# Performance work log

Measured on AMD Instinct MI355X. Metric: run time of the kernel, lower is better.

## Reference

```python
import jax, jax.numpy as jnp
import numpy as np

WS = 3          # window size (odd)
NH = 8          # num heads
EPS = 1e-5      # LayerNorm eps (torch default)


def _ln(x, g, b):
    mu = x.mean(-1, keepdims=True)
    var = ((x - mu) ** 2).mean(-1, keepdims=True)
    return (x - mu) / jnp.sqrt(var + EPS) * g + b


def _neighbors(x, ws):
    # x: [B,D,H,W,C] -> [B,D,H,W,ws^3,C] zero-padded cubic neighborhoods
    B, D, H, W, C = x.shape
    r = ws // 2
    xp = jnp.pad(x, ((0, 0), (r, r), (r, r), (r, r), (0, 0)))
    slabs = [xp[:, i:i + D, j:j + H, k:k + W, :]
             for i in range(ws) for j in range(ws) for k in range(ws)]
    return jnp.stack(slabs, axis=4)


def _mask(D, H, W, ws):
    # True for valid (in-bounds, non-center) neighbors: [D,H,W,ws^3]
    r = ws // 2
    valid = jnp.pad(jnp.ones((D, H, W), dtype=bool), ((r, r), (r, r), (r, r)))
    slabs = [valid[i:i + D, j:j + H, k:k + W]
             for i in range(ws) for j in range(ws) for k in range(ws)]
    m = jnp.stack(slabs, axis=3)
    center = r * ws * ws + r * ws + r  # self voxel is masked out
    return m.at[..., center].set(False)


def setup_inputs() -> dict:
    key = jax.random.key(0)
    ks = jax.random.split(key, 18)
    B, D, H, W, C = 2, 16, 16, 16, 256
    F = 4 * C
    s = 0.02
    inp = {
        "x": jax.random.normal(ks[0], (B, D, H, W, C), jnp.float32),
        "Wq": jax.random.normal(ks[1], (C, C), jnp.float32) * s,
        "bq": jnp.zeros((C,), jnp.float32),
        "Wk": jax.random.normal(ks[2], (C, C), jnp.float32) * s,
        "bk": jnp.zeros((C,), jnp.float32),
        "Wv": jax.random.normal(ks[3], (C, C), jnp.float32) * s,
        "bv": jnp.zeros((C,), jnp.float32),
        "Wo": jax.random.normal(ks[4], (C, C), jnp.float32) * s,
        "bo": jnp.zeros((C,), jnp.float32),
        "g1": jnp.ones((C,), jnp.float32),
        "b1": jnp.zeros((C,), jnp.float32),
        "g2": jnp.ones((C,), jnp.float32),
        "b2": jnp.zeros((C,), jnp.float32),
        "W1": jax.random.normal(ks[5], (C, F), jnp.float32) * s,
        "bf1": jnp.zeros((F,), jnp.float32),
        "W2": jax.random.normal(ks[6], (F, C), jnp.float32) * s,
        "bf2": jnp.zeros((C,), jnp.float32),
    }
    return inp


def reference(x, Wq, bq, Wk, bk, Wv, bv, Wo, bo, g1, b1, g2, b2, W1, bf1, W2, bf2):
    B, D, H, W, C = x.shape
    ws, nh = WS, NH
    hd = C // nh
    K = ws ** 3

    nb = _neighbors(x, ws)                                   # [B,D,H,W,K,C]
    m = _mask(D, H, W, ws)                                   # [D,H,W,K]

    tn = _ln(x, g1, b1)                                      # norm1 on target only
    q = (tn @ Wq + bq).reshape(B, D, H, W, nh, hd)
    k = (nb @ Wk + bk).reshape(B, D, H, W, K, nh, hd)        # keys from RAW neighbors
    v = (nb @ Wv + bv).reshape(B, D, H, W, K, nh, hd)

    scale = hd ** -0.5
    scores = jnp.einsum('bpqrne,bpqrkne->bpqrnk', q, k) * scale  # [B,D,H,W,nh,K]
    mb = m[None, :, :, :, None, :]
    scores = jnp.where(mb, scores, -jnp.inf)
    attn = jax.nn.softmax(scores, axis=-1)
    attn = jnp.where(jnp.isnan(attn), jnp.zeros_like(attn), attn)

    ao = jnp.einsum('bpqrnk,bpqrkne->bpqrne', attn, v).reshape(B, D, H, W, C)
    ao = ao @ Wo + bo

    t = x + ao                                                # residual (dropout = eval identity)
    h = jax.nn.gelu(_ln(t, g2, b2) @ W1 + bf1, approximate=False) @ W2 + bf2
    return t + h
```

## Files before the change

kernel.cpp:

```cpp
#include <hip/hip_runtime.h>

typedef __bf16 bf16x8 __attribute__((ext_vector_type(8)));
typedef float f32x4 __attribute__((ext_vector_type(4)));

#define DEV static __device__ __forceinline__

DEV unsigned short f2b(float f){
    unsigned int u = __float_as_uint(f);
    u += 0x7fffu + ((u >> 16) & 1u);
    return (unsigned short)(u >> 16);
}
DEV float b2f(unsigned short h){ return __uint_as_float(((unsigned int)h) << 16); }
DEV float blo(unsigned int u){ return __uint_as_float(u << 16); }
DEV float bhi(unsigned int u){ return __uint_as_float(u & 0xffff0000u); }
DEV float gelu_f(float x){ return 0.5f * x * (1.0f + erff(x * 0.7071067811865476f)); }

DEV void gload16(const unsigned short* g, unsigned short* l){
    __builtin_amdgcn_global_load_lds(
        (const __attribute__((address_space(1))) void*)g,
        (__attribute__((address_space(3))) void*)l, 16, 0, 0);
}

static constexpr int NROW = 8192;
static constexpr int C    = 256;
static constexpr int F    = 1024;
static constexpr float ATT_SCALE = 0.17677669529663688f;

__global__ __launch_bounds__(256)
void prep_ln_kernel(const float* __restrict__ Wq, const float* __restrict__ Wk,
                    const float* __restrict__ Wv, const float* __restrict__ Wo,
                    const float* __restrict__ W1, const float* __restrict__ W2,
                    const float* __restrict__ bq, const float* __restrict__ bk,
                    const float* __restrict__ bv,
                    unsigned short* __restrict__ WQT, unsigned short* __restrict__ WKT,
                    unsigned short* __restrict__ WVT, unsigned short* __restrict__ WOT,
                    unsigned short* __restrict__ W1T, unsigned short* __restrict__ W2T,
                    float* __restrict__ bqkv,
                    const float* __restrict__ x, const float* __restrict__ g1,
                    const float* __restrict__ b1,
                    unsigned short* __restrict__ tn, unsigned short* __restrict__ xb)
{
    const int tid = threadIdx.x;
    if (blockIdx.x < 192) {
        __shared__ unsigned short T[64][66];
        const int t = blockIdx.x;
        const float* src; unsigned short* dst;
        int ldw, ldt, r0, c0; float sc = 1.0f;
        if (t < 64) {
            const int m = t >> 4, sub = t & 15;
            src = (m == 0) ? Wq : (m == 1) ? Wk : (m == 2) ? Wv : Wo;
            dst = (m == 0) ? WQT : (m == 1) ? WKT : (m == 2) ? WVT : WOT;
            if (m == 0) sc = ATT_SCALE;
            ldw = 256; ldt = 256;
            r0 = (sub >> 2) * 64; c0 = (sub & 3) * 64;
        } else if (t < 128) {
            const int sub = t - 64;
            src = W1; dst = W1T; ldw = 1024; ldt = 256;
            r0 = (sub >> 4) * 64; c0 = (sub & 15) * 64;
        } else {
            const int sub = t - 128;
            src = W2; dst = W2T; ldw = 256; ldt = 1024;
            r0 = (sub >> 2) * 64; c0 = (sub & 3) * 64;
        }
        #pragma unroll
        for (int i = 0; i < 16; ++i) {
            const int rl = i * 4 + (tid >> 6), cl = tid & 63;
            T[rl][cl] = f2b(src[(size_t)(r0 + rl) * ldw + c0 + cl] * sc);
        }
        __syncthreads();
        #pragma unroll
        for (int j = 0; j < 16; ++j) {
            const int cl = j * 4 + (tid >> 6), rl = tid & 63;
            dst[(size_t)(c0 + cl) * ldt + r0 + rl] = T[rl][cl];
        }
    } else if (blockIdx.x == 192) {
        #pragma unroll
        for (int i = 0; i < 3; ++i) {
            const int v = i * 256 + tid;
            bqkv[v] = (v < 256) ? bq[v] * ATT_SCALE
                    : (v < 512) ? bk[v - 256] : bv[v - 512];
        }
    } else {
        const int row  = (blockIdx.x - 193) * 4 + (tid >> 6);
        const int lane = tid & 63;
        float4 v = ((const float4*)(x + (size_t)row * C))[lane];
        float s = v.x + v.y + v.z + v.w;
        #pragma unroll
        for (int m = 32; m >= 1; m >>= 1) s += __shfl_xor(s, m);
        const float mean = s * (1.0f / 256.0f);
        const float d0 = v.x - mean, d1 = v.y - mean, d2 = v.z - mean, d3 = v.w - mean;
        float s2 = d0 * d0 + d1 * d1 + d2 * d2 + d3 * d3;
        #pragma unroll
        for (int m = 32; m >= 1; m >>= 1) s2 += __shfl_xor(s2, m);
        const float rstd = rsqrtf(s2 * (1.0f / 256.0f) + 1e-5f);
        float4 gg = ((const float4*)g1)[lane];
        float4 bb = ((const float4*)b1)[lane];
        ushort4 o = { f2b(d0 * rstd * gg.x + bb.x), f2b(d1 * rstd * gg.y + bb.y),
                      f2b(d2 * rstd * gg.z + bb.z), f2b(d3 * rstd * gg.w + bb.w) };
        ((ushort4*)(tn + (size_t)row * C))[lane] = o;
        ushort4 xo = { f2b(v.x), f2b(v.y), f2b(v.z), f2b(v.w) };
        ((ushort4*)(xb + (size_t)row * C))[lane] = xo;
    }
}

__global__ __launch_bounds__(256)
void ln_kernel(const float* __restrict__ X, const float* __restrict__ g,
               const float* __restrict__ bta, unsigned short* __restrict__ OUT)
{
    const int row  = blockIdx.x * 4 + (threadIdx.x >> 6);
    const int lane = threadIdx.x & 63;
    float4 v = ((const float4*)(X + (size_t)row * C))[lane];
    float s = v.x + v.y + v.z + v.w;
    #pragma unroll
    for (int m = 32; m >= 1; m >>= 1) s += __shfl_xor(s, m);
    const float mean = s * (1.0f / 256.0f);
    const float d0 = v.x - mean, d1 = v.y - mean, d2 = v.z - mean, d3 = v.w - mean;
    float s2 = d0 * d0 + d1 * d1 + d2 * d2 + d3 * d3;
    #pragma unroll
    for (int m = 32; m >= 1; m >>= 1) s2 += __shfl_xor(s2, m);
    const float rstd = rsqrtf(s2 * (1.0f / 256.0f) + 1e-5f);
    float4 gg = ((const float4*)g)[lane];
    float4 bb = ((const float4*)bta)[lane];
    ushort4 o = { f2b(d0 * rstd * gg.x + bb.x), f2b(d1 * rstd * gg.y + bb.y),
                  f2b(d2 * rstd * gg.z + bb.z), f2b(d3 * rstd * gg.w + bb.w) };
    ((ushort4*)(OUT + (size_t)row * C))[lane] = o;
}

template<int K, int MODE>
DEV void gemm_body(const unsigned short* __restrict__ A, int m0,
                   const unsigned short* __restrict__ BTt,
                   const float* __restrict__ biast,
                   const float* __restrict__ res, void* __restrict__ outp,
                   int ldo, int ocol0,
                   unsigned short (&As)[2][4096], unsigned short (&Bs)[2][4096])
{
    constexpr int BK = 64, NKT = K / BK;
    const int tid  = threadIdx.x;
    const int lane = tid & 63, wid = tid >> 6;
    const int srow = tid >> 3;
    const int schk = (tid & 7) ^ (srow & 7);

    const unsigned short* Ag = A   + (size_t)(m0 + srow) * K + schk * 8;
    const unsigned short* Bg = BTt + (size_t)srow        * K + schk * 8;

    const int wbase = __builtin_amdgcn_readfirstlane(wid) * 512;

    gload16(Ag,          &As[0][wbase]);
    gload16(Ag + 32 * K, &As[0][wbase + 2048]);
    gload16(Bg,          &Bs[0][wbase]);
    gload16(Bg + 32 * K, &Bs[0][wbase + 2048]);
    __syncthreads();

    f32x4 acc[4] = {};
    const int lr = lane & 15, lk = lane >> 4;
    const int sw = lr & 7;

    for (int kt = 0; kt < NKT; ++kt) {
        if (kt + 1 < NKT) {
            const int nb = (kt + 1) & 1;
            gload16(Ag + (kt + 1) * BK,          &As[nb][wbase]);
            gload16(Ag + 32 * K + (kt + 1) * BK, &As[nb][wbase + 2048]);
            gload16(Bg + (kt + 1) * BK,          &Bs[nb][wbase]);
            gload16(Bg + 32 * K + (kt + 1) * BK, &Bs[nb][wbase + 2048]);
        }
        const unsigned short* as = As[kt & 1];
        const unsigned short* bs = Bs[kt & 1];
        #pragma unroll
        for (int s = 0; s < 2; ++s) {
            const int c16 = (s * 4 + lk) ^ sw;
            bf16x8 bfr = *reinterpret_cast<const bf16x8*>(&bs[(wid * 16 + lr) * 64 + c16 * 8]);
            #pragma unroll
            for (int m = 0; m < 4; ++m) {
                bf16x8 afr = *reinterpret_cast<const bf16x8*>(&as[(m * 16 + lr) * 64 + c16 * 8]);
                acc[m] = __builtin_amdgcn_mfma_f32_16x16x32_bf16(afr, bfr, acc[m], 0, 0, 0);
            }
        }
        if (kt + 1 < NKT) __syncthreads();
    }

    const int col  = ocol0 + wid * 16 + lr;
    const float bcol = biast[wid * 16 + lr];
    #pragma unroll
    for (int m = 0; m < 4; ++m) {
        #pragma unroll
        for (int r = 0; r < 4; ++r) {
            const int row = m0 + m * 16 + lk * 4 + r;
            float v = acc[m][r] + bcol;
            if (MODE == 0) {
                ((unsigned short*)outp)[(size_t)row * ldo + col] = f2b(v);
            } else if (MODE == 1) {
                ((unsigned short*)outp)[(size_t)row * ldo + col] = f2b(gelu_f(v));
            } else {
                v += res[(size_t)row * ldo + col];
                ((float*)outp)[(size_t)row * ldo + col] = v;
            }
        }
    }
}

template<int K, int MODE>
DEV void gemm_bodyN128(const unsigned short* __restrict__ A, int m0,
                       const unsigned short* __restrict__ BTt,
                       const float* __restrict__ biast,
                       const float* __restrict__ res, void* __restrict__ outp,
                       int ldo, int ocol0,
                       unsigned short (&As)[2][4096], unsigned short (&Bs)[2][8192])
{
    constexpr int BK = 64, NKT = K / BK;
    const int tid  = threadIdx.x;
    const int lane = tid & 63, wid = tid >> 6;
    const int srow = tid >> 3;
    const int schk = (tid & 7) ^ (srow & 7);

    const unsigned short* Ag = A   + (size_t)(m0 + srow) * K + schk * 8;
    const unsigned short* Bg = BTt + (size_t)srow        * K + schk * 8;

    const int wbase = __builtin_amdgcn_readfirstlane(wid) * 512;

    gload16(Ag,          &As[0][wbase]);
    gload16(Ag + 32 * K, &As[0][wbase + 2048]);
    #pragma unroll
    for (int i = 0; i < 4; ++i)
        gload16(Bg + (size_t)(32 * i) * K, &Bs[0][i * 2048 + wbase]);
    __syncthreads();

    f32x4 acc[4][2] = {};
    const int lr = lane & 15, lk = lane >> 4;
    const int sw = lr & 7;
    const int brow = wid * 32;

    for (int kt = 0; kt < NKT; ++kt) {
        if (kt + 1 < NKT) {
            const int nb = (kt + 1) & 1;
            gload16(Ag + (kt + 1) * BK,          &As[nb][wbase]);
            gload16(Ag + 32 * K + (kt + 1) * BK, &As[nb][wbase + 2048]);
            #pragma unroll
            for (int i = 0; i < 4; ++i)
                gload16(Bg + (size_t)(32 * i) * K + (kt + 1) * BK, &Bs[nb][i * 2048 + wbase]);
        }
        const unsigned short* as = As[kt & 1];
        const unsigned short* bs = Bs[kt & 1];
        #pragma unroll
        for (int ks = 0; ks < 2; ++ks) {
            const int c16 = (ks * 4 + lk) ^ sw;
            bf16x8 af[4], bf[2];
            #pragma unroll
            for (int m = 0; m < 4; ++m)
                af[m] = *reinterpret_cast<const bf16x8*>(&as[(m * 16 + lr) * 64 + c16 * 8]);
            #pragma unroll
            for (int n = 0; n < 2; ++n)
                bf[n] = *reinterpret_cast<const bf16x8*>(&bs[(brow + n * 16 + lr) * 64 + c16 * 8]);
            #pragma unroll
            for (int m = 0; m < 4; ++m)
                #pragma unroll
                for (int n = 0; n < 2; ++n)
                    acc[m][n] = __builtin_amdgcn_mfma_f32_16x16x32_bf16(af[m], bf[n], acc[m][n], 0, 0, 0);
        }
        if (kt + 1 < NKT) __syncthreads();
    }

    #pragma unroll
    for (int n = 0; n < 2; ++n) {
        const int cl  = brow + n * 16 + lr;
        const int col = ocol0 + cl;
        const float bcol = biast[cl];
        #pragma unroll
        for (int m = 0; m < 4; ++m) {
            #pragma unroll
            for (int r = 0; r < 4; ++r) {
                const int row = m0 + m * 16 + lk * 4 + r;
                float v = acc[m][n][r] + bcol;
                if (MODE == 0) {
                    ((unsigned short*)outp)[(size_t)row * ldo + col] = f2b(v);
                } else if (MODE == 1) {
                    ((unsigned short*)outp)[(size_t)row * ldo + col] = f2b(gelu_f(v));
                } else {
                    v += res[(size_t)row * ldo + col];
                    ((float*)outp)[(size_t)row * ldo + col] = v;
                }
            }
        }
    }
}

template<int NC, int TS>
DEV void tile_map(int& m0, int& n0){
    const int nwg = gridDim.x;
    const int lin = blockIdx.x;
    const int tile = (lin & 7) * (nwg >> 3) + (lin >> 3);
    m0 = (tile / NC) * TS;
    n0 = (tile % NC) * TS;
}
template<int NC, int TSM, int TSN>
DEV void tile_map2(int& m0, int& n0){
    const int nwg = gridDim.x;
    const int lin = blockIdx.x;
    const int tile = (lin & 7) * (nwg >> 3) + (lin >> 3);
    m0 = (tile / NC) * TSM;
    n0 = (tile % NC) * TSN;
}

__global__ __launch_bounds__(256, 3)
void qkv_kernel(const unsigned short* __restrict__ tn,
                const unsigned short* __restrict__ xb,
                const unsigned short* __restrict__ WT,
                const float* __restrict__ bqkv,
                unsigned short* __restrict__ QKV)
{
    __shared__ unsigned short As[2][4096], Bs[2][8192];
    int m0, n0; tile_map2<6, 64, 128>(m0, n0);
    const unsigned short* A = (n0 < 256) ? tn : xb;
    gemm_bodyN128<256, 0>(A, m0, WT + (size_t)n0 * 256,
                          bqkv + n0, nullptr, QKV, 768, n0, As, Bs);
}

__global__ __launch_bounds__(256, 3)
void w1_kernel(const unsigned short* __restrict__ tn2,
               const unsigned short* __restrict__ W1T,
               const float* __restrict__ bf1,
               unsigned short* __restrict__ Hb)
{
    __shared__ unsigned short As[2][4096], Bs[2][8192];
    int m0, n0; tile_map2<8, 64, 128>(m0, n0);
    gemm_bodyN128<256, 1>(tn2, m0, W1T + (size_t)n0 * 256,
                          bf1 + n0, nullptr, Hb, 1024, n0, As, Bs);
}

template<int K, int MODE, int NC>
__global__ __launch_bounds__(256)
void gemm_kernel(const unsigned short* __restrict__ A,
                 const unsigned short* __restrict__ BT,
                 const float* __restrict__ bias,
                 const float* __restrict__ res,
                 void* __restrict__ outp, int ldo)
{
    __shared__ unsigned short As[2][4096], Bs[2][4096];
    int m0, n0; tile_map<NC, 64>(m0, n0);
    gemm_body<K, MODE>(A, m0, BT + (size_t)n0 * K,
                       bias + n0, res, outp, ldo, n0, As, Bs);
}

DEV float dot8(uint4 u, const float* q){
    float s;
    s = q[0] * blo(u.x);          s = fmaf(q[1], bhi(u.x), s);
    s = fmaf(q[2], blo(u.y), s);  s = fmaf(q[3], bhi(u.y), s);
    s = fmaf(q[4], blo(u.z), s);  s = fmaf(q[5], bhi(u.z), s);
    s = fmaf(q[6], blo(u.w), s);  s = fmaf(q[7], bhi(u.w), s);
    return s;
}

__global__ __launch_bounds__(256, 4)
void attn_kernel(const unsigned short* __restrict__ QKV,
                 unsigned short* __restrict__ AO)
{
    const int t   = blockIdx.x * 256 + threadIdx.x;
    const int vox = t >> 5;
    const int ch  = (t & 31) * 8;
    const int d = (vox >> 8) & 15, h = (vox >> 4) & 15, w = vox & 15;

    float q[8];
    {
        uint4 u = *reinterpret_cast<const uint4*>(&QKV[(size_t)vox * 768 + ch]);
        q[0]=blo(u.x); q[1]=bhi(u.x); q[2]=blo(u.y); q[3]=bhi(u.y);
        q[4]=blo(u.z); q[5]=bhi(u.z); q[6]=blo(u.w); q[7]=bhi(u.w);
    }

    float mrun = -1e30f, z = 0.0f;
    float acc[8] = {};

    #pragma unroll
    for (int g = 0; g < 3; ++g) {
        const int di = g - 1;
        const int nd = d + di;
        int r9[9];
        unsigned vm = 0;
        #pragma unroll
        for (int j = 0; j < 9; ++j) {
            const int hi2 = j / 3 - 1, wi = j % 3 - 1;
            const int nh = h + hi2, nw = w + wi;
            const bool valid = !(di == 0 && hi2 == 0 && wi == 0) &&
                               ((unsigned)nd < 16u) && ((unsigned)nh < 16u) &&
                               ((unsigned)nw < 16u);
            r9[j] = valid ? ((vox & 4096) | (nd << 8) | (nh << 4) | nw) : vox;
            vm |= (unsigned)valid << j;
        }

        uint4 ku[9];
        #pragma unroll
        for (int j = 0; j < 9; ++j)
            ku[j] = *reinterpret_cast<const uint4*>(
                &QKV[(size_t)r9[j] * 768 + 256 + ch]);

        float s9[9];
        #pragma unroll
        for (int j = 0; j < 9; ++j) {
            float s = dot8(ku[j], q);
            s += __shfl_xor(s, 1);
            s += __shfl_xor(s, 2);
            s9[j] = ((vm >> j) & 1u) ? s : -INFINITY;
        }

        float gm = s9[0];
        #pragma unroll
        for (int j = 1; j < 9; ++j) gm = fmaxf(gm, s9[j]);
        const float nm = fmaxf(mrun, gm);
        const float rs = __expf(mrun - nm);
        mrun = nm;
        z *= rs;
        #pragma unroll
        for (int i = 0; i < 8; ++i) acc[i] *= rs;

        uint4 vu[9];
        #pragma unroll
        for (int j = 0; j < 9; ++j)
            vu[j] = *reinterpret_cast<const uint4*>(
                &QKV[(size_t)r9[j] * 768 + 512 + ch]);

        #pragma unroll
        for (int j = 0; j < 9; ++j) {
            const float p = __expf(s9[j] - nm);
            z += p;
            const uint4 u = vu[j];
            acc[0] = fmaf(p, blo(u.x), acc[0]); acc[1] = fmaf(p, bhi(u.x), acc[1]);
            acc[2] = fmaf(p, blo(u.y), acc[2]); acc[3] = fmaf(p, bhi(u.y), acc[3]);
            acc[4] = fmaf(p, blo(u.z), acc[4]); acc[5] = fmaf(p, bhi(u.z), acc[5]);
            acc[6] = fmaf(p, blo(u.w), acc[6]); acc[7] = fmaf(p, bhi(u.w), acc[7]);
        }
    }

    const float inv = 1.0f / z;
    uint4 o;
    o.x = (unsigned)f2b(acc[0] * inv) | ((unsigned)f2b(acc[1] * inv) << 16);
    o.y = (unsigned)f2b(acc[2] * inv) | ((unsigned)f2b(acc[3] * inv) << 16);
    o.z = (unsigned)f2b(acc[4] * inv) | ((unsigned)f2b(acc[5] * inv) << 16);
    o.w = (unsigned)f2b(acc[6] * inv) | ((unsigned)f2b(acc[7] * inv) << 16);
    *reinterpret_cast<uint4*>(&AO[(size_t)vox * C + ch]) = o;
}

extern "C" void kernel_launch(void* const* d_in, const int* in_sizes, int n_in,
                              void* d_out, int out_size, void* d_ws, size_t ws_size,
                              hipStream_t stream)
{
    const float* x   = (const float*)d_in[0];
    const float* Wq  = (const float*)d_in[1];
    const float* bq  = (const float*)d_in[2];
    const float* Wk  = (const float*)d_in[3];
    const float* bk  = (const float*)d_in[4];
    const float* Wv  = (const float*)d_in[5];
    const float* bv  = (const float*)d_in[6];
    const float* Wo  = (const float*)d_in[7];
    const float* bo  = (const float*)d_in[8];
    const float* g1  = (const float*)d_in[9];
    const float* b1  = (const float*)d_in[10];
    const float* g2  = (const float*)d_in[11];
    const float* b2  = (const float*)d_in[12];
    const float* W1  = (const float*)d_in[13];
    const float* bf1 = (const float*)d_in[14];
    const float* W2  = (const float*)d_in[15];
    const float* bf2 = (const float*)d_in[16];

    char* ws = (char*)d_ws;
    size_t o = 0;
    unsigned short* WQT = (unsigned short*)(ws + o); o += (size_t)256 * 256 * 2;
    unsigned short* WKT = (unsigned short*)(ws + o); o += (size_t)256 * 256 * 2;
    unsigned short* WVT = (unsigned short*)(ws + o); o += (size_t)256 * 256 * 2;
    unsigned short* WOT = (unsigned short*)(ws + o); o += (size_t)256 * 256 * 2;
    unsigned short* W1T = (unsigned short*)(ws + o); o += (size_t)256 * 1024 * 2;
    unsigned short* W2T = (unsigned short*)(ws + o); o += (size_t)1024 * 256 * 2;
    float*          bqkv= (float*)(ws + o);          o += (size_t)768 * 4;
    unsigned short* tn  = (unsigned short*)(ws + o); o += (size_t)NROW * C * 2;
    unsigned short* xb  = (unsigned short*)(ws + o); o += (size_t)NROW * C * 2;
    unsigned short* QKVb= (unsigned short*)(ws + o); o += (size_t)NROW * 768 * 2;
    unsigned short* AOb = (unsigned short*)(ws + o); o += (size_t)NROW * C * 2;
    float*          Tf  = (float*)(ws + o);          o += (size_t)NROW * C * 4;
    unsigned short* tn2 = (unsigned short*)(ws + o); o += (size_t)NROW * C * 2;
    unsigned short* Hb  = (unsigned short*)(ws + o); o += (size_t)NROW * F * 2;

    prep_ln_kernel<<<193 + NROW / 4, 256, 0, stream>>>(Wq, Wk, Wv, Wo, W1, W2, bq, bk, bv,
                                                       WQT, WKT, WVT, WOT, W1T, W2T, bqkv,
                                                       x, g1, b1, tn, xb);

    qkv_kernel<<<(NROW / 64) * 6, 256, 0, stream>>>(tn, xb, WQT, bqkv, QKVb);

    attn_kernel<<<NROW * 32 / 256, 256, 0, stream>>>(QKVb, AOb);

    gemm_kernel<256, 2, 4><<<(NROW / 64) * 4, 256, 0, stream>>>(AOb, WOT, bo, x, Tf, 256);

    ln_kernel<<<NROW / 4, 256, 0, stream>>>(Tf, g2, b2, tn2);

    w1_kernel<<<(NROW / 64) * 8, 256, 0, stream>>>(tn2, W1T, bf1, Hb);

    gemm_kernel<1024, 2, 4><<<(NROW / 64) * 4, 256, 0, stream>>>(Hb, W2T, bf2, Tf, (float*)d_out, 256);
}
```

Before: 74.97 us.

## Fuse Wo projection GEMM with residual add and LayerNorm2 into one kernel

Replaces the separate Wo GEMM and LayerNorm kernels with a single kernel. Each block computes a 32-row by full-256-column output tile, adds bias and residual, then reduces row statistics in registers and shared memory to emit both Tf and the normalized bf16 tn2. This removes one launch and the re-read of Tf from global memory, at the cost of fewer blocks (256) and larger shared memory per block, which limits occupancy. The attention kernel also issues its K and V loads together for each slice to overlap more memory latency, which raises register pressure.

```diff
diff --git a/kernel.cpp b/kernel.cpp
--- a/kernel.cpp
+++ b/kernel.cpp
@@ -103,29 +103,6 @@
     }
 }
 
-__global__ __launch_bounds__(256)
-void ln_kernel(const float* __restrict__ X, const float* __restrict__ g,
-               const float* __restrict__ bta, unsigned short* __restrict__ OUT)
-{
-    const int row  = blockIdx.x * 4 + (threadIdx.x >> 6);
-    const int lane = threadIdx.x & 63;
-    float4 v = ((const float4*)(X + (size_t)row * C))[lane];
-    float s = v.x + v.y + v.z + v.w;
-    #pragma unroll
-    for (int m = 32; m >= 1; m >>= 1) s += __shfl_xor(s, m);
-    const float mean = s * (1.0f / 256.0f);
-    const float d0 = v.x - mean, d1 = v.y - mean, d2 = v.z - mean, d3 = v.w - mean;
-    float s2 = d0 * d0 + d1 * d1 + d2 * d2 + d3 * d3;
-    #pragma unroll
-    for (int m = 32; m >= 1; m >>= 1) s2 += __shfl_xor(s2, m);
-    const float rstd = rsqrtf(s2 * (1.0f / 256.0f) + 1e-5f);
-    float4 gg = ((const float4*)g)[lane];
-    float4 bb = ((const float4*)bta)[lane];
-    ushort4 o = { f2b(d0 * rstd * gg.x + bb.x), f2b(d1 * rstd * gg.y + bb.y),
-                  f2b(d2 * rstd * gg.z + bb.z), f2b(d3 * rstd * gg.w + bb.w) };
-    ((ushort4*)(OUT + (size_t)row * C))[lane] = o;
-}
-
 template<int K, int MODE>
 DEV void gemm_body(const unsigned short* __restrict__ A, int m0,
                    const unsigned short* __restrict__ BTt,
@@ -340,6 +317,146 @@
                        bias + n0, res, outp, ldo, n0, As, Bs);
 }
 
+__global__ __launch_bounds__(256, 2)
+void wo_ln_kernel(const unsigned short* __restrict__ AOb,
+                  const unsigned short* __restrict__ WOT,
+                  const float* __restrict__ bo,
+                  const float* __restrict__ x,
+                  const float* __restrict__ g2, const float* __restrict__ b2,
+                  float* __restrict__ Tf,
+                  unsigned short* __restrict__ tn2)
+{
+    __shared__ unsigned short As[2][2048];
+    __shared__ unsigned short Bs[2][16384];
+    __shared__ float2 red[4][32];
+
+    const int lin = blockIdx.x;
+    const int m0  = ((lin & 7) * (gridDim.x >> 3) + (lin >> 3)) * 32;
+
+    const int tid  = threadIdx.x;
+    const int lane = tid & 63, wid = tid >> 6;
+    const int srow = tid >> 3;
+    const int schk = (tid & 7) ^ (srow & 7);
+
+    const unsigned short* Ag = AOb + (size_t)(m0 + srow) * 256 + schk * 8;
+    const unsigned short* Bg = WOT + (size_t)srow        * 256 + schk * 8;
+
+    const int wbase = __builtin_amdgcn_readfirstlane(wid) * 512;
+
+    gload16(Ag, &As[0][wbase]);
+    #pragma unroll
+    for (int i = 0; i < 8; ++i)
+        gload16(Bg + (size_t)(32 * i) * 256, &Bs[0][i * 2048 + wbase]);
+    __syncthreads();
+
+    f32x4 acc[2][4] = {};
+    const int lr = lane & 15, lk = lane >> 4;
+    const int sw = lr & 7;
+    const int wc = wid * 64;
+
+    for (int kt = 0; kt < 4; ++kt) {
+        if (kt < 3) {
+            const int nb = (kt + 1) & 1;
+            gload16(Ag + (kt + 1) * 64, &As[nb][wbase]);
+            #pragma unroll
+            for (int i = 0; i < 8; ++i)
+                gload16(Bg + (size_t)(32 * i) * 256 + (kt + 1) * 64, &Bs[nb][i * 2048 + wbase]);
+        }
+        const unsigned short* as = As[kt & 1];
+        const unsigned short* bs = Bs[kt & 1];
+        #pragma unroll
+        for (int ks = 0; ks < 2; ++ks) {
+            const int c16 = (ks * 4 + lk) ^ sw;
+            bf16x8 af[2], bf[4];
+            #pragma unroll
+            for (int m = 0; m < 2; ++m)
+                af[m] = *reinterpret_cast<const bf16x8*>(&as[(m * 16 + lr) * 64 + c16 * 8]);
+            #pragma unroll
+            for (int n = 0; n < 4; ++n)
+                bf[n] = *reinterpret_cast<const bf16x8*>(&bs[(wc + n * 16 + lr) * 64 + c16 * 8]);
+            #pragma unroll
+            for (int m = 0; m < 2; ++m)
+                #pragma unroll
+                for (int n = 0; n < 4; ++n)
+                    acc[m][n] = __builtin_amdgcn_mfma_f32_16x16x32_bf16(af[m], bf[n], acc[m][n], 0, 0, 0);
+        }
+        if (kt < 3) __syncthreads();
+    }
+
+    #pragma unroll
+    for (int n = 0; n < 4; ++n) {
+        const int col = wc + n * 16 + lr;
+        const float bcol = bo[col];
+        #pragma unroll
+        for (int m = 0; m < 2; ++m) {
+            #pragma unroll
+            for (int r = 0; r < 4; ++r) {
+                const int row = m0 + m * 16 + lk * 4 + r;
+                acc[m][n][r] += bcol + x[(size_t)row * 256 + col];
+            }
+        }
+    }
+
+    float s1[2][4], s2[2][4];
+    #pragma unroll
+    for (int m = 0; m < 2; ++m)
+        #pragma unroll
+        for (int r = 0; r < 4; ++r) {
+            float a = 0.f, b = 0.f;
+            #pragma unroll
+            for (int n = 0; n < 4; ++n) { const float v = acc[m][n][r]; a += v; b += v * v; }
+            s1[m][r] = a; s2[m][r] = b;
+        }
+    #pragma unroll
+    for (int mask = 1; mask <= 8; mask <<= 1)
+        #pragma unroll
+        for (int m = 0; m < 2; ++m)
+            #pragma unroll
+            for (int r = 0; r < 4; ++r) {
+                s1[m][r] += __shfl_xor(s1[m][r], mask);
+                s2[m][r] += __shfl_xor(s2[m][r], mask);
+            }
+    if (lr == 0) {
+        #pragma unroll
+        for (int m = 0; m < 2; ++m)
+            #pragma unroll
+            for (int r = 0; r < 4; ++r)
+                red[wid][m * 16 + lk * 4 + r] = make_float2(s1[m][r], s2[m][r]);
+    }
+    __syncthreads();
+
+    float mean[2][4], rstd[2][4];
+    #pragma unroll
+    for (int m = 0; m < 2; ++m)
+        #pragma unroll
+        for (int r = 0; r < 4; ++r) {
+            const int rl = m * 16 + lk * 4 + r;
+            float a = 0.f, b = 0.f;
+            #pragma unroll
+            for (int w4 = 0; w4 < 4; ++w4) { const float2 p = red[w4][rl]; a += p.x; b += p.y; }
+            const float mu = a * (1.0f / 256.0f);
+            mean[m][r] = mu;
+            rstd[m][r] = rsqrtf(b * (1.0f / 256.0f) - mu * mu + 1e-5f);
+        }
+
+    #pragma unroll
+    for (int n = 0; n < 4; ++n) {
+        const int col = wc + n * 16 + lr;
+        const float gc = g2[col], bc = b2[col];
+        #pragma unroll
+        for (int m = 0; m < 2; ++m) {
+            #pragma unroll
+            for (int r = 0; r < 4; ++r) {
+                const int row = m0 + m * 16 + lk * 4 + r;
+                const float v = acc[m][n][r];
+                Tf[(size_t)row * 256 + col] = v;
+                tn2[(size_t)row * 256 + col] =
+                    f2b((v - mean[m][r]) * rstd[m][r] * gc + bc);
+            }
+        }
+    }
+}
+
 DEV float dot8(uint4 u, const float* q){
     float s;
     s = q[0] * blo(u.x);          s = fmaf(q[1], bhi(u.x), s);
@@ -372,8 +489,8 @@
     for (int g = 0; g < 3; ++g) {
         const int di = g - 1;
         const int nd = d + di;
-        int r9[9];
         unsigned vm = 0;
+        uint4 ku[9], vu[9];
         #pragma unroll
         for (int j = 0; j < 9; ++j) {
             const int hi2 = j / 3 - 1, wi = j % 3 - 1;
@@ -381,15 +498,12 @@
             const bool valid = !(di == 0 && hi2 == 0 && wi == 0) &&
                                ((unsigned)nd < 16u) && ((unsigned)nh < 16u) &&
                                ((unsigned)nw < 16u);
-            r9[j] = valid ? ((vox & 4096) | (nd << 8) | (nh << 4) | nw) : vox;
+            const int r = valid ? ((vox & 4096) | (nd << 8) | (nh << 4) | nw) : vox;
             vm |= (unsigned)valid << j;
-        }
-
-        uint4 ku[9];
-        #pragma unroll
-        for (int j = 0; j < 9; ++j)
-            ku[j] = *reinterpret_cast<const uint4*>(
-                &QKV[(size_t)r9[j] * 768 + 256 + ch]);
+            const unsigned short* base = &QKV[(size_t)r * 768 + 256 + ch];
+            ku[j] = *reinterpret_cast<const uint4*>(base);
+            vu[j] = *reinterpret_cast<const uint4*>(base + 256);
+        }
 
         float s9[9];
         #pragma unroll
@@ -409,12 +523,6 @@
         z *= rs;
         #pragma unroll
         for (int i = 0; i < 8; ++i) acc[i] *= rs;
-
-        uint4 vu[9];
-        #pragma unroll
-        for (int j = 0; j < 9; ++j)
-            vu[j] = *reinterpret_cast<const uint4*>(
-                &QKV[(size_t)r9[j] * 768 + 512 + ch]);
 
         #pragma unroll
         for (int j = 0; j < 9; ++j) {
@@ -484,9 +592,7 @@
 
     attn_kernel<<<NROW * 32 / 256, 256, 0, stream>>>(QKVb, AOb);
 
-    gemm_kernel<256, 2, 4><<<(NROW / 64) * 4, 256, 0, stream>>>(AOb, WOT, bo, x, Tf, 256);
-
-    ln_kernel<<<NROW / 4, 256, 0, stream>>>(Tf, g2, b2, tn2);
+    wo_ln_kernel<<<NROW / 32, 256, 0, stream>>>(AOb, WOT, bo, x, g2, b2, Tf, tn2);
 
     w1_kernel<<<(NROW / 64) * 8, 256, 0, stream>>>(tn2, W1T, bf1, Hb);
 
```

Measured after the change: 74.53 us. No clear change (-0.6%).
